# Optimization experiments

Measured on AMD Instinct MI355X. Metric: run time of the kernel, lower is better.

Reference implementation:

```python
import jax, jax.numpy as jnp
import numpy as np

D_MODEL = 2048
N_HEADS = 16
HEAD_DIM = D_MODEL // N_HEADS  # 128
ROPE_BASE = 10000.0


def _rope_cos_sin(T, hd, dtype):
    inv_freq = 1.0 / (ROPE_BASE ** (jnp.arange(0, hd, 2, dtype=jnp.float32) / hd))
    freqs = jnp.arange(T, dtype=jnp.float32)[:, None] * inv_freq[None, :]  # [T, hd/2]
    emb = jnp.concatenate([freqs, freqs], axis=-1)  # [T, hd]
    return jnp.cos(emb).astype(dtype), jnp.sin(emb).astype(dtype)


def _rotate_half(x):
    h = x.shape[-1] // 2
    return jnp.concatenate([-x[..., h:], x[..., :h]], axis=-1)


def setup_inputs() -> dict:
    key = jax.random.key(0)
    k1, k2, k3, k4 = jax.random.split(key, 4)
    B, T = 2, 2048
    x = jax.random.normal(k1, (B, T, D_MODEL), dtype=jnp.float32)
    # Linear weights stored as [in, out] so y = x @ W (same math as torch's x @ W.T)
    Wqkv = jax.random.normal(k2, (D_MODEL, 3 * D_MODEL), dtype=jnp.float32) * (D_MODEL ** -0.5)
    Wproj = jax.random.normal(k3, (D_MODEL, D_MODEL), dtype=jnp.float32) * (D_MODEL ** -0.5)
    bproj = jax.random.normal(k4, (D_MODEL,), dtype=jnp.float32) * 0.01
    # additive causal mask: 0 on/below diagonal, -1e9 above
    causal = jnp.tril(jnp.ones((T, T), dtype=bool))
    mask = jnp.where(causal, 0.0, -1e9).astype(jnp.float32)
    return {"x": x, "Wqkv": Wqkv, "Wproj": Wproj, "bproj": bproj, "mask": mask}


def reference(x, Wqkv, Wproj, bproj, mask):
    B, T, D = x.shape
    H, hd = N_HEADS, HEAD_DIM
    scale = hd ** -0.5

    qkv = x @ Wqkv  # [B, T, 3D]
    q, k, v = jnp.split(qkv, 3, axis=-1)
    q = q.reshape(B, T, H, hd).transpose(0, 2, 1, 3)  # [B, H, T, hd]
    k = k.reshape(B, T, H, hd).transpose(0, 2, 1, 3)
    v = v.reshape(B, T, H, hd).transpose(0, 2, 1, 3)

    cos, sin = _rope_cos_sin(T, hd, x.dtype)  # [T, hd]
    q = q * cos + _rotate_half(q) * sin
    k = k * cos + _rotate_half(k) * sin

    attn = jnp.einsum('bhtd,bhsd->bhts', q, k) * scale  # [B, H, T, T]
    attn = attn + mask  # broadcast [T, T] over (B, H)
    attn = jax.nn.softmax(attn, axis=-1)
    out = jnp.einsum('bhts,bhsd->bhtd', attn, v)  # [B, H, T, hd]
    out = out.transpose(0, 2, 1, 3).reshape(B, T, D)
    return out @ Wproj + bproj
```

## Files before the change

### kernel.cpp

```cpp
#include <hip/hip_runtime.h>
#include <cstdint>

#define BB 2
#define TT 2048
#define DM 2048
#define NH 16
#define HD 128
#define QKVN 6144

using f32x4   = __attribute__((ext_vector_type(4))) float;
using bf16x8  = __attribute__((ext_vector_type(8))) __bf16;
using ushort8 = __attribute__((ext_vector_type(8))) unsigned short;

static __device__ __forceinline__ unsigned short f2bf(float f) {
    uint32_t u = __builtin_bit_cast(uint32_t, f);
    u += 0x7FFFu + ((u >> 16) & 1u);
    return (unsigned short)(u >> 16);
}
static __device__ __forceinline__ float bf2f(unsigned short h) {
    return __builtin_bit_cast(float, ((uint32_t)h) << 16);
}

#define GLOAD16(SRC, DST)                                               \
    __builtin_amdgcn_global_load_lds(                                   \
        (const __attribute__((address_space(1))) void*)(SRC),           \
        (__attribute__((address_space(3))) void*)(DST), 16, 0, 0)

__global__ __launch_bounds__(256) void k_split(const float* __restrict__ in,
                                               unsigned short* __restrict__ hi,
                                               unsigned short* __restrict__ lo,
                                               int n4) {
    int i = blockIdx.x * 256 + threadIdx.x;
    if (i >= n4) return;
    float4 v = reinterpret_cast<const float4*>(in)[i];
    ushort4 h, l;
    h.x = f2bf(v.x); l.x = f2bf(v.x - bf2f(h.x));
    h.y = f2bf(v.y); l.y = f2bf(v.y - bf2f(h.y));
    h.z = f2bf(v.z); l.z = f2bf(v.z - bf2f(h.z));
    h.w = f2bf(v.w); l.w = f2bf(v.w - bf2f(h.w));
    reinterpret_cast<ushort4*>(hi)[i] = h;
    reinterpret_cast<ushort4*>(lo)[i] = l;
}

__global__ __launch_bounds__(256) void k_tsplit(const float* __restrict__ W,
                                                unsigned short* __restrict__ th,
                                                int K, int N) {
    __shared__ float tile[32][33];
    int bn = blockIdx.x * 32, bk = blockIdx.y * 32;
    int tx = threadIdx.x, ty = threadIdx.y;
#pragma unroll
    for (int r = 0; r < 4; r++)
        tile[ty + 8 * r][tx] = W[(size_t)(bk + ty + 8 * r) * N + bn + tx];
    __syncthreads();
#pragma unroll
    for (int r = 0; r < 4; r++) {
        float v = tile[tx][ty + 8 * r];
        int row = bn + ty + 8 * r, col = bk + tx;
        th[(size_t)row * K + col] = f2bf(v);
    }
}

template <int EPI>
__global__ __launch_bounds__(512, 2) void k_gemm(
    const unsigned short* __restrict__ Ah, const unsigned short* __restrict__ Al,
    const unsigned short* __restrict__ Bh,
    unsigned short* __restrict__ Ch,
    float* __restrict__ Cf, const float* __restrict__ bias,
    int M, int N, int K) {
    __shared__ __align__(16) unsigned short sAh[2][16384];
    __shared__ __align__(16) unsigned short sAl[2][16384];
    __shared__ __align__(16) unsigned short sBh[2][8192];

    const int nwg = gridDim.x * gridDim.y;
    const int L = blockIdx.y * gridDim.x + blockIdx.x;
    const int logical = (L & 7) * (nwg >> 3) + (L >> 3);
    const int bx = logical % gridDim.x, by = logical / gridDim.x;

    const int tid = threadIdx.x;
    const int wave = tid >> 6, lane = tid & 63;
    const int g = lane >> 4, r16 = lane & 15;
    const int arow0 = by * 256, bcol0 = bx * 128;
    const int wr = (wave >> 1) * 64, wc = (wave & 1) * 64;
    const int sw8 = r16 & 7;

    const int srow = tid >> 3;
    const int scol = ((tid & 7) ^ (srow & 7)) << 3;

    f32x4 acc[4][4];
#pragma unroll
    for (int m = 0; m < 4; m++)
#pragma unroll
        for (int n = 0; n < 4; n++) acc[m][n] = (f32x4){0.f, 0.f, 0.f, 0.f};

    const int NT = K >> 6;

    auto stageA_hi = [&](int buf, int tk) {
        const size_t kof = (size_t)tk * 64 + scol;
#pragma unroll
        for (int i = 0; i < 4; i++)
            GLOAD16(Ah + (size_t)(arow0 + i * 64 + srow) * K + kof,
                    &sAh[buf][(i * 512 + tid) * 8]);
    };
    auto stageA_lo = [&](int buf, int tk) {
        const size_t kof = (size_t)tk * 64 + scol;
#pragma unroll
        for (int i = 0; i < 4; i++)
            GLOAD16(Al + (size_t)(arow0 + i * 64 + srow) * K + kof,
                    &sAl[buf][(i * 512 + tid) * 8]);
    };
    auto stageB = [&](int buf, int tk) {
        const size_t kof = (size_t)tk * 64 + scol;
#pragma unroll
        for (int i = 0; i < 2; i++)
            GLOAD16(Bh + (size_t)(bcol0 + i * 64 + srow) * K + kof,
                    &sBh[buf][(i * 512 + tid) * 8]);
    };

    auto rdA = [&](int buf, int m, int co, bf16x8& h, bf16x8& l) {
        int ro = (wr + m * 16 + r16) * 64 + co;
        h = __builtin_bit_cast(bf16x8, *(const ushort8*)&sAh[buf][ro]);
        l = __builtin_bit_cast(bf16x8, *(const ushort8*)&sAl[buf][ro]);
    };
    auto rdB = [&](int buf, int n, int co) {
        int ro = (wc + n * 16 + r16) * 64 + co;
        return __builtin_bit_cast(bf16x8, *(const ushort8*)&sBh[buf][ro]);
    };

    stageA_hi(0, 0); stageA_lo(0, 0); stageB(0, 0);

    int cur = 0;
    for (int t = 0; t < NT; ++t) {
        asm volatile("s_waitcnt vmcnt(0)" ::: "memory");
        __builtin_amdgcn_s_barrier();
        const bool pf = (t + 1 < NT);
        const int nb = cur ^ 1;
        const int co0 = (g ^ sw8) << 3, co1 = ((4 + g) ^ sw8) << 3;

        bf16x8 ah0[4], al0[4], bh0[4], ah1[4], al1[4], bh1[4];

#pragma unroll
        for (int n = 0; n < 4; n++) bh0[n] = rdB(cur, n, co0);
        rdA(cur, 0, co0, ah0[0], al0[0]);
        rdA(cur, 1, co0, ah0[1], al0[1]);
        __builtin_amdgcn_sched_barrier(0);
        rdA(cur, 2, co0, ah0[2], al0[2]);
        rdA(cur, 3, co0, ah0[3], al0[3]);
        __builtin_amdgcn_sched_barrier(0);
        if (pf) stageA_hi(nb, t + 1);
        asm volatile("s_waitcnt lgkmcnt(4)" ::: "memory");
        __builtin_amdgcn_sched_barrier(0);
        __builtin_amdgcn_s_setprio(1);
#pragma unroll
        for (int m = 0; m < 2; m++)
#pragma unroll
            for (int n = 0; n < 4; n++) {
                acc[m][n] = __builtin_amdgcn_mfma_f32_16x16x32_bf16(ah0[m], bh0[n], acc[m][n], 0, 0, 0);
                acc[m][n] = __builtin_amdgcn_mfma_f32_16x16x32_bf16(al0[m], bh0[n], acc[m][n], 0, 0, 0);
            }
        __builtin_amdgcn_s_setprio(0);
        __builtin_amdgcn_s_barrier();

        rdA(cur, 0, co1, ah1[0], al1[0]);
        rdA(cur, 1, co1, ah1[1], al1[1]);
        __builtin_amdgcn_sched_barrier(0);
        if (pf) stageA_lo(nb, t + 1);
        asm volatile("s_waitcnt lgkmcnt(4)" ::: "memory");
        __builtin_amdgcn_sched_barrier(0);
        __builtin_amdgcn_s_setprio(1);
#pragma unroll
        for (int m = 2; m < 4; m++)
#pragma unroll
            for (int n = 0; n < 4; n++) {
                acc[m][n] = __builtin_amdgcn_mfma_f32_16x16x32_bf16(ah0[m], bh0[n], acc[m][n], 0, 0, 0);
                acc[m][n] = __builtin_amdgcn_mfma_f32_16x16x32_bf16(al0[m], bh0[n], acc[m][n], 0, 0, 0);
            }
        __builtin_amdgcn_s_setprio(0);
        __builtin_amdgcn_s_barrier();

#pragma unroll
        for (int n = 0; n < 4; n++) bh1[n] = rdB(cur, n, co1);
        __builtin_amdgcn_sched_barrier(0);
        rdA(cur, 2, co1, ah1[2], al1[2]);
        rdA(cur, 3, co1, ah1[3], al1[3]);
        __builtin_amdgcn_sched_barrier(0);
        if (pf) stageB(nb, t + 1);
        asm volatile("s_waitcnt lgkmcnt(4)" ::: "memory");
        __builtin_amdgcn_sched_barrier(0);
        __builtin_amdgcn_s_setprio(1);
#pragma unroll
        for (int m = 0; m < 2; m++)
#pragma unroll
            for (int n = 0; n < 4; n++) {
                acc[m][n] = __builtin_amdgcn_mfma_f32_16x16x32_bf16(ah1[m], bh1[n], acc[m][n], 0, 0, 0);
                acc[m][n] = __builtin_amdgcn_mfma_f32_16x16x32_bf16(al1[m], bh1[n], acc[m][n], 0, 0, 0);
            }
        __builtin_amdgcn_s_setprio(0);
        __builtin_amdgcn_s_barrier();

        asm volatile("s_waitcnt lgkmcnt(0)" ::: "memory");
        __builtin_amdgcn_sched_barrier(0);
        __builtin_amdgcn_s_setprio(1);
#pragma unroll
        for (int m = 2; m < 4; m++)
#pragma unroll
            for (int n = 0; n < 4; n++) {
                acc[m][n] = __builtin_amdgcn_mfma_f32_16x16x32_bf16(ah1[m], bh1[n], acc[m][n], 0, 0, 0);
                acc[m][n] = __builtin_amdgcn_mfma_f32_16x16x32_bf16(al1[m], bh1[n], acc[m][n], 0, 0, 0);
            }
        __builtin_amdgcn_s_setprio(0);
        cur ^= 1;
    }

#pragma unroll
    for (int m = 0; m < 4; m++)
#pragma unroll
        for (int n = 0; n < 4; n++) {
            int col = bcol0 + wc + n * 16 + r16;
#pragma unroll
            for (int j = 0; j < 4; j++) {
                int row = arow0 + wr + m * 16 + g * 4 + j;
                float v = acc[m][n][j];
                if (EPI == 0) {
                    Ch[(size_t)row * N + col] = f2bf(v);
                } else {
                    Cf[(size_t)row * N + col] = v + bias[col];
                }
            }
        }
}

__global__ __launch_bounds__(256) void k_rope(unsigned short* __restrict__ qh) {
    __shared__ float row[4096];
    __shared__ float cs[64], sn[64];
    const int rb = blockIdx.x;
    const int t = rb & (TT - 1);
    const int tid = threadIdx.x;
    if (tid < 64) {
        float invf = 1.0f / powf(10000.0f, (float)tid * (1.0f / 64.0f));
        float s, c;
        sincosf((float)t * invf, &s, &c);
        cs[tid] = c; sn[tid] = s;
    }
    const size_t base = (size_t)rb * QKVN;
#pragma unroll
    for (int i = 0; i < 2; i++) {
        int c0 = (tid + i * 256) * 8;
        ushort8 h = *(const ushort8*)&qh[base + c0];
#pragma unroll
        for (int e = 0; e < 8; e++) row[c0 + e] = bf2f(h[e]);
    }
    __syncthreads();
#pragma unroll
    for (int i = 0; i < 2; i++) {
        int c0 = (tid + i * 256) * 8;
        int d0 = c0 & 127;
        ushort8 h;
#pragma unroll
        for (int e = 0; e < 8; e++) {
            int c = c0 + e, d = d0 + e;
            float x = row[c];
            float xr = (d < 64) ? -row[c + 64] : row[c - 64];
            float v = x * cs[d & 63] + xr * sn[d & 63];
            h[e] = f2bf(v);
        }
        *(ushort8*)&qh[base + c0] = h;
    }
}

__global__ __launch_bounds__(128) void k_vt(const unsigned short* __restrict__ qkvh,
                                            unsigned short* __restrict__ vt) {
    const int bh = blockIdx.x;
    const int tc = blockIdx.y;
    const int d = threadIdx.x;
    const int b = bh >> 4, h = bh & 15;
    unsigned short buf[64];
    const size_t src0 = ((size_t)(b * TT + tc * 64)) * QKVN + 4096 + h * 128 + d;
#pragma unroll
    for (int ttt = 0; ttt < 64; ttt++) buf[ttt] = qkvh[src0 + (size_t)ttt * QKVN];
    const size_t dst = ((size_t)bh * 128 + d) * TT + tc * 64;
#pragma unroll
    for (int i = 0; i < 8; i++)
        *(ushort8*)&vt[dst + i * 8] = *(const ushort8*)&buf[i * 8];
}

__global__ __launch_bounds__(256) void k_flash(const unsigned short* __restrict__ qkvh,
                                               const unsigned short* __restrict__ vt,
                                               unsigned short* __restrict__ aoh,
                                               unsigned short* __restrict__ aol) {
    __shared__ unsigned short sK[2][64 * 128];
    __shared__ unsigned short sV[2][128 * 64];
    __shared__ unsigned short sP[4][16 * 64];

    const int L = blockIdx.y * gridDim.x + blockIdx.x;
    const int logical = (L & 7) * 128 + (L >> 3);
    const int bh = logical >> 5;
    const int qb = 31 - (logical & 31);
    const int b = bh >> 4, h = bh & 15;

    const int tid = threadIdx.x, wave = tid >> 6, lane = tid & 63;
    const int g = lane >> 4, r16 = lane & 15;
    const float scale = 0.08838834764831845f;

    bf16x8 qf[4];
    {
        const int qrow = qb * 64 + wave * 16 + r16;
        const size_t qbase = ((size_t)(b * TT) + qrow) * QKVN + h * 128;
#pragma unroll
        for (int kk = 0; kk < 4; kk++) {
            ushort8 u = *(const ushort8*)&qkvh[qbase + kk * 32 + g * 8];
            ushort8 o;
#pragma unroll
            for (int e = 0; e < 8; e++) o[e] = f2bf(bf2f(u[e]) * scale);
            qf[kk] = __builtin_bit_cast(bf16x8, o);
        }
    }

    f32x4 oacc[8];
#pragma unroll
    for (int n = 0; n < 8; n++) oacc[n] = (f32x4){0.f, 0.f, 0.f, 0.f};
    float mrun[4], lrun[4];
#pragma unroll
    for (int j = 0; j < 4; j++) { mrun[j] = -1e30f; lrun[j] = 0.f; }

    const int k_row_st = wave * 4 + (lane >> 4);
    const int v_row_st = wave * 8 + (lane >> 3);
    const int lidx = wave * 512 + lane * 8;

    auto stage = [&](int buf, int kb) {
#pragma unroll
        for (int i = 0; i < 4; i++) {
            int krow = i * 16 + k_row_st;
            int kcol = ((lane & 15) ^ (krow & 7)) << 3;
            GLOAD16(qkvh + ((size_t)(b * TT + kb * 64 + krow)) * QKVN + 2048 + h * 128 + kcol,
                    &sK[buf][i * 2048 + lidx]);
            int vrow = i * 32 + v_row_st;
            int vcol = ((lane & 7) ^ (vrow & 7)) << 3;
            GLOAD16(vt + ((size_t)bh * 128 + vrow) * TT + kb * 64 + vcol,
                    &sV[buf][i * 2048 + lidx]);
        }
    };

    const int nkb = qb + 1;
    int cur = 0;
    stage(0, 0);

    for (int kb = 0; kb < nkb; kb++) {
        __syncthreads();
        if (kb + 1 < nkb) stage(cur ^ 1, kb + 1);

        f32x4 sacc[4];
#pragma unroll
        for (int n = 0; n < 4; n++) sacc[n] = (f32x4){0.f, 0.f, 0.f, 0.f};
#pragma unroll
        for (int n = 0; n < 4; n++) {
            const int krow = n * 16 + r16;
            const int rbase = krow * 128;
            const int sw = krow & 7;
#pragma unroll
            for (int kk = 0; kk < 4; kk++) {
                int slot = (kk * 4 + g) ^ sw;
                bf16x8 kf = __builtin_bit_cast(bf16x8, *(const ushort8*)&sK[cur][rbase + slot * 8]);
                sacc[n] = __builtin_amdgcn_mfma_f32_16x16x32_bf16(qf[kk], kf, sacc[n], 0, 0, 0);
            }
        }

        const int key0 = kb * 64;
#pragma unroll
        for (int j = 0; j < 4; j++) {
            const int prow = g * 4 + j;
            const int qg = qb * 64 + wave * 16 + prow;
            float s0 = sacc[0][j], s1 = sacc[1][j], s2 = sacc[2][j], s3 = sacc[3][j];
            if (kb == qb) {
                if (key0 + r16 > qg)      s0 = -1e30f;
                if (key0 + 16 + r16 > qg) s1 = -1e30f;
                if (key0 + 32 + r16 > qg) s2 = -1e30f;
                if (key0 + 48 + r16 > qg) s3 = -1e30f;
            }
            float tmax = fmaxf(fmaxf(s0, s1), fmaxf(s2, s3));
#pragma unroll
            for (int off = 8; off >= 1; off >>= 1) tmax = fmaxf(tmax, __shfl_xor(tmax, off));
            float mnew = fmaxf(mrun[j], tmax);
            float corr = __expf(mrun[j] - mnew);
            float p0 = __expf(s0 - mnew), p1 = __expf(s1 - mnew);
            float p2 = __expf(s2 - mnew), p3 = __expf(s3 - mnew);
            float rs = (p0 + p1) + (p2 + p3);
#pragma unroll
            for (int off = 8; off >= 1; off >>= 1) rs += __shfl_xor(rs, off);
            lrun[j] = lrun[j] * corr + rs;
            mrun[j] = mnew;
#pragma unroll
            for (int n = 0; n < 8; n++) oacc[n][j] *= corr;
            const int pb = prow * 64, sw = prow & 7, e = r16 & 7, hi2 = (r16 >> 3);
            sP[wave][pb + (((0 + hi2) ^ sw) << 3) + e] = f2bf(p0);
            sP[wave][pb + (((2 + hi2) ^ sw) << 3) + e] = f2bf(p1);
            sP[wave][pb + (((4 + hi2) ^ sw) << 3) + e] = f2bf(p2);
            sP[wave][pb + (((6 + hi2) ^ sw) << 3) + e] = f2bf(p3);
        }

#pragma unroll
        for (int kk = 0; kk < 2; kk++) {
            const int slot = (kk * 4 + g) ^ (r16 & 7);
            bf16x8 pf = __builtin_bit_cast(bf16x8, *(const ushort8*)&sP[wave][r16 * 64 + slot * 8]);
#pragma unroll
            for (int n = 0; n < 8; n++) {
                const int d = n * 16 + r16;
                bf16x8 vf = __builtin_bit_cast(bf16x8, *(const ushort8*)&sV[cur][d * 64 + slot * 8]);
                oacc[n] = __builtin_amdgcn_mfma_f32_16x16x32_bf16(pf, vf, oacc[n], 0, 0, 0);
            }
        }
        cur ^= 1;
    }

#pragma unroll
    for (int j = 0; j < 4; j++) {
        float inv = 1.0f / lrun[j];
        int qg = qb * 64 + wave * 16 + g * 4 + j;
        size_t obase = ((size_t)(b * TT) + qg) * DM + h * 128;
#pragma unroll
        for (int n = 0; n < 8; n++) {
            float v = oacc[n][j] * inv;
            unsigned short hh = f2bf(v);
            aoh[obase + n * 16 + r16] = hh;
            aol[obase + n * 16 + r16] = f2bf(v - bf2f(hh));
        }
    }
}

extern "C" void kernel_launch(void* const* d_in, const int* in_sizes, int n_in,
                              void* d_out, int out_size, void* d_ws, size_t ws_size,
                              hipStream_t stream) {
    const float* x = (const float*)d_in[0];
    const float* Wqkv = (const float*)d_in[1];
    const float* Wproj = (const float*)d_in[2];
    const float* bproj = (const float*)d_in[3];

    uint8_t* w = (uint8_t*)d_ws;
    auto alloc = [&](size_t bytes) { uint8_t* p = w; w += bytes; return p; };
    unsigned short* xh   = (unsigned short*)alloc(8388608ull * 2);
    unsigned short* xl   = (unsigned short*)alloc(8388608ull * 2);
    unsigned short* wqh  = (unsigned short*)alloc(12582912ull * 2);
    unsigned short* wph  = (unsigned short*)alloc(4194304ull * 2);
    unsigned short* qkvh = (unsigned short*)alloc(25165824ull * 2);
    unsigned short* vtp  = (unsigned short*)alloc(8388608ull * 2);
    unsigned short* aoh  = (unsigned short*)alloc(8388608ull * 2);
    unsigned short* aol  = (unsigned short*)alloc(8388608ull * 2);

    k_split<<<dim3(8192), dim3(256), 0, stream>>>(x, xh, xl, 2097152);
    k_tsplit<<<dim3(192, 64), dim3(32, 8), 0, stream>>>(Wqkv, wqh, 2048, 6144);
    k_tsplit<<<dim3(64, 64), dim3(32, 8), 0, stream>>>(Wproj, wph, 2048, 2048);
    k_gemm<0><<<dim3(48, 16), dim3(512), 0, stream>>>(xh, xl, wqh,
                                                      qkvh, nullptr, nullptr,
                                                      4096, 6144, 2048);
    k_rope<<<dim3(4096), dim3(256), 0, stream>>>(qkvh);
    k_vt<<<dim3(32, 32), dim3(128), 0, stream>>>(qkvh, vtp);
    k_flash<<<dim3(32, 32), dim3(256), 0, stream>>>(qkvh, vtp, aoh, aol);
    k_gemm<1><<<dim3(16, 16), dim3(512), 0, stream>>>(aoh, aol, wph,
                                                      nullptr, (float*)d_out, bproj,
                                                      4096, 2048, 2048);
}
```

Before: 559.6 us.

## Load GEMM A operand directly to registers and drop lo-split for projection

The GEMM no longer stages the A operand (hi/lo bf16 halves) through LDS. Each wave loads its A fragments straight from global memory into registers, one k-tile ahead, and only B stays double-buffered in shared memory. Most intra-iteration barriers are removed and the vmcnt waits are relaxed. Separately, the attention output is written only as a single bf16 (no lo residual), and the output projection GEMM runs without the split term, halving its MFMA work. The risks are lower accuracy in the projection and uncoalesced per-lane global loads for A, with more register pressure.

```diff
diff --git a/kernel.cpp b/kernel.cpp
--- a/kernel.cpp
+++ b/kernel.cpp
@@ -60,15 +60,13 @@
     }
 }
 
-template <int EPI>
+template <int EPI, int SPLIT>
 __global__ __launch_bounds__(512, 2) void k_gemm(
     const unsigned short* __restrict__ Ah, const unsigned short* __restrict__ Al,
     const unsigned short* __restrict__ Bh,
     unsigned short* __restrict__ Ch,
     float* __restrict__ Cf, const float* __restrict__ bias,
     int M, int N, int K) {
-    __shared__ __align__(16) unsigned short sAh[2][16384];
-    __shared__ __align__(16) unsigned short sAl[2][16384];
     __shared__ __align__(16) unsigned short sBh[2][8192];
 
     const int nwg = gridDim.x * gridDim.y;
@@ -86,6 +84,11 @@
     const int srow = tid >> 3;
     const int scol = ((tid & 7) ^ (srow & 7)) << 3;
 
+    size_t aBase[4];
+#pragma unroll
+    for (int m = 0; m < 4; m++)
+        aBase[m] = (size_t)(arow0 + wr + m * 16 + r16) * K + g * 8;
+
     f32x4 acc[4][4];
 #pragma unroll
     for (int m = 0; m < 4; m++)
@@ -94,20 +97,6 @@
 
     const int NT = K >> 6;
 
-    auto stageA_hi = [&](int buf, int tk) {
-        const size_t kof = (size_t)tk * 64 + scol;
-#pragma unroll
-        for (int i = 0; i < 4; i++)
-            GLOAD16(Ah + (size_t)(arow0 + i * 64 + srow) * K + kof,
-                    &sAh[buf][(i * 512 + tid) * 8]);
-    };
-    auto stageA_lo = [&](int buf, int tk) {
-        const size_t kof = (size_t)tk * 64 + scol;
-#pragma unroll
-        for (int i = 0; i < 4; i++)
-            GLOAD16(Al + (size_t)(arow0 + i * 64 + srow) * K + kof,
-                    &sAl[buf][(i * 512 + tid) * 8]);
-    };
     auto stageB = [&](int buf, int tk) {
         const size_t kof = (size_t)tk * 64 + scol;
 #pragma unroll
@@ -115,99 +104,97 @@
             GLOAD16(Bh + (size_t)(bcol0 + i * 64 + srow) * K + kof,
                     &sBh[buf][(i * 512 + tid) * 8]);
     };
-
-    auto rdA = [&](int buf, int m, int co, bf16x8& h, bf16x8& l) {
-        int ro = (wr + m * 16 + r16) * 64 + co;
-        h = __builtin_bit_cast(bf16x8, *(const ushort8*)&sAh[buf][ro]);
-        l = __builtin_bit_cast(bf16x8, *(const ushort8*)&sAl[buf][ro]);
-    };
-    auto rdB = [&](int buf, int n, int co) {
-        int ro = (wc + n * 16 + r16) * 64 + co;
+    auto rdB = [&](int buf, int n, int slot) {
+        int ro = (wc + n * 16 + r16) * 64 + ((slot ^ sw8) << 3);
         return __builtin_bit_cast(bf16x8, *(const ushort8*)&sBh[buf][ro]);
     };
 
-    stageA_hi(0, 0); stageA_lo(0, 0); stageB(0, 0);
+    bf16x8 a0h[4], a0l[4], a1h[4], a1l[4];
+    auto loadA0 = [&](int kcol) {
+#pragma unroll
+        for (int m = 0; m < 4; m++) {
+            a0h[m] = __builtin_bit_cast(bf16x8, *(const ushort8*)(Ah + aBase[m] + kcol));
+            if (SPLIT) a0l[m] = __builtin_bit_cast(bf16x8, *(const ushort8*)(Al + aBase[m] + kcol));
+        }
+    };
+    auto loadA1 = [&](int kcol) {
+#pragma unroll
+        for (int m = 0; m < 4; m++) {
+            a1h[m] = __builtin_bit_cast(bf16x8, *(const ushort8*)(Ah + aBase[m] + kcol + 32));
+            if (SPLIT) a1l[m] = __builtin_bit_cast(bf16x8, *(const ushort8*)(Al + aBase[m] + kcol + 32));
+        }
+    };
+
+    stageB(0, 0);
+    loadA0(0);
+    loadA1(0);
 
     int cur = 0;
     for (int t = 0; t < NT; ++t) {
-        asm volatile("s_waitcnt vmcnt(0)" ::: "memory");
+        if (SPLIT) asm volatile("s_waitcnt vmcnt(16)" ::: "memory");
+        else       asm volatile("s_waitcnt vmcnt(8)" ::: "memory");
         __builtin_amdgcn_s_barrier();
         const bool pf = (t + 1 < NT);
         const int nb = cur ^ 1;
-        const int co0 = (g ^ sw8) << 3, co1 = ((4 + g) ^ sw8) << 3;
-
-        bf16x8 ah0[4], al0[4], bh0[4], ah1[4], al1[4], bh1[4];
-
-#pragma unroll
-        for (int n = 0; n < 4; n++) bh0[n] = rdB(cur, n, co0);
-        rdA(cur, 0, co0, ah0[0], al0[0]);
-        rdA(cur, 1, co0, ah0[1], al0[1]);
-        __builtin_amdgcn_sched_barrier(0);
-        rdA(cur, 2, co0, ah0[2], al0[2]);
-        rdA(cur, 3, co0, ah0[3], al0[3]);
-        __builtin_amdgcn_sched_barrier(0);
-        if (pf) stageA_hi(nb, t + 1);
-        asm volatile("s_waitcnt lgkmcnt(4)" ::: "memory");
+        const int nkcol = (t + 1) * 64;
+
+        bf16x8 bh0[4], bh1[4];
+#pragma unroll
+        for (int n = 0; n < 4; n++) bh0[n] = rdB(cur, n, g);
+#pragma unroll
+        for (int n = 0; n < 4; n++) bh1[n] = rdB(cur, n, 4 + g);
+        if (pf) stageB(nb, t + 1);
         __builtin_amdgcn_sched_barrier(0);
         __builtin_amdgcn_s_setprio(1);
 #pragma unroll
         for (int m = 0; m < 2; m++)
 #pragma unroll
             for (int n = 0; n < 4; n++) {
-                acc[m][n] = __builtin_amdgcn_mfma_f32_16x16x32_bf16(ah0[m], bh0[n], acc[m][n], 0, 0, 0);
-                acc[m][n] = __builtin_amdgcn_mfma_f32_16x16x32_bf16(al0[m], bh0[n], acc[m][n], 0, 0, 0);
+                acc[m][n] = __builtin_amdgcn_mfma_f32_16x16x32_bf16(a0h[m], bh0[n], acc[m][n], 0, 0, 0);
+                if (SPLIT)
+                    acc[m][n] = __builtin_amdgcn_mfma_f32_16x16x32_bf16(a0l[m], bh0[n], acc[m][n], 0, 0, 0);
             }
         __builtin_amdgcn_s_setprio(0);
-        __builtin_amdgcn_s_barrier();
-
-        rdA(cur, 0, co1, ah1[0], al1[0]);
-        rdA(cur, 1, co1, ah1[1], al1[1]);
-        __builtin_amdgcn_sched_barrier(0);
-        if (pf) stageA_lo(nb, t + 1);
-        asm volatile("s_waitcnt lgkmcnt(4)" ::: "memory");
-        __builtin_amdgcn_sched_barrier(0);
+        __builtin_amdgcn_sched_barrier(0);
+
         __builtin_amdgcn_s_setprio(1);
 #pragma unroll
         for (int m = 2; m < 4; m++)
 #pragma unroll
             for (int n = 0; n < 4; n++) {
-                acc[m][n] = __builtin_amdgcn_mfma_f32_16x16x32_bf16(ah0[m], bh0[n], acc[m][n], 0, 0, 0);
-                acc[m][n] = __builtin_amdgcn_mfma_f32_16x16x32_bf16(al0[m], bh0[n], acc[m][n], 0, 0, 0);
+                acc[m][n] = __builtin_amdgcn_mfma_f32_16x16x32_bf16(a0h[m], bh0[n], acc[m][n], 0, 0, 0);
+                if (SPLIT)
+                    acc[m][n] = __builtin_amdgcn_mfma_f32_16x16x32_bf16(a0l[m], bh0[n], acc[m][n], 0, 0, 0);
             }
         __builtin_amdgcn_s_setprio(0);
-        __builtin_amdgcn_s_barrier();
-
-#pragma unroll
-        for (int n = 0; n < 4; n++) bh1[n] = rdB(cur, n, co1);
-        __builtin_amdgcn_sched_barrier(0);
-        rdA(cur, 2, co1, ah1[2], al1[2]);
-        rdA(cur, 3, co1, ah1[3], al1[3]);
-        __builtin_amdgcn_sched_barrier(0);
-        if (pf) stageB(nb, t + 1);
-        asm volatile("s_waitcnt lgkmcnt(4)" ::: "memory");
+        __builtin_amdgcn_sched_barrier(0);
+
+        if (pf) loadA0(nkcol);
         __builtin_amdgcn_sched_barrier(0);
         __builtin_amdgcn_s_setprio(1);
 #pragma unroll
         for (int m = 0; m < 2; m++)
 #pragma unroll
             for (int n = 0; n < 4; n++) {
-                acc[m][n] = __builtin_amdgcn_mfma_f32_16x16x32_bf16(ah1[m], bh1[n], acc[m][n], 0, 0, 0);
-                acc[m][n] = __builtin_amdgcn_mfma_f32_16x16x32_bf16(al1[m], bh1[n], acc[m][n], 0, 0, 0);
+                acc[m][n] = __builtin_amdgcn_mfma_f32_16x16x32_bf16(a1h[m], bh1[n], acc[m][n], 0, 0, 0);
+                if (SPLIT)
+                    acc[m][n] = __builtin_amdgcn_mfma_f32_16x16x32_bf16(a1l[m], bh1[n], acc[m][n], 0, 0, 0);
             }
         __builtin_amdgcn_s_setprio(0);
-        __builtin_amdgcn_s_barrier();
-
-        asm volatile("s_waitcnt lgkmcnt(0)" ::: "memory");
-        __builtin_amdgcn_sched_barrier(0);
+        __builtin_amdgcn_sched_barrier(0);
+
         __builtin_amdgcn_s_setprio(1);
 #pragma unroll
         for (int m = 2; m < 4; m++)
 #pragma unroll
             for (int n = 0; n < 4; n++) {
-                acc[m][n] = __builtin_amdgcn_mfma_f32_16x16x32_bf16(ah1[m], bh1[n], acc[m][n], 0, 0, 0);
-                acc[m][n] = __builtin_amdgcn_mfma_f32_16x16x32_bf16(al1[m], bh1[n], acc[m][n], 0, 0, 0);
+                acc[m][n] = __builtin_amdgcn_mfma_f32_16x16x32_bf16(a1h[m], bh1[n], acc[m][n], 0, 0, 0);
+                if (SPLIT)
+                    acc[m][n] = __builtin_amdgcn_mfma_f32_16x16x32_bf16(a1l[m], bh1[n], acc[m][n], 0, 0, 0);
             }
         __builtin_amdgcn_s_setprio(0);
+        __builtin_amdgcn_sched_barrier(0);
+        if (pf) loadA1(nkcol);
         cur ^= 1;
     }
 
@@ -285,8 +272,7 @@
 
 __global__ __launch_bounds__(256) void k_flash(const unsigned short* __restrict__ qkvh,
                                                const unsigned short* __restrict__ vt,
-                                               unsigned short* __restrict__ aoh,
-                                               unsigned short* __restrict__ aol) {
+                                               unsigned short* __restrict__ aoh) {
     __shared__ unsigned short sK[2][64 * 128];
     __shared__ unsigned short sV[2][128 * 64];
     __shared__ unsigned short sP[4][16 * 64];
@@ -417,12 +403,8 @@
         int qg = qb * 64 + wave * 16 + g * 4 + j;
         size_t obase = ((size_t)(b * TT) + qg) * DM + h * 128;
 #pragma unroll
-        for (int n = 0; n < 8; n++) {
-            float v = oacc[n][j] * inv;
-            unsigned short hh = f2bf(v);
-            aoh[obase + n * 16 + r16] = hh;
-            aol[obase + n * 16 + r16] = f2bf(v - bf2f(hh));
-        }
+        for (int n = 0; n < 8; n++)
+            aoh[obase + n * 16 + r16] = f2bf(oacc[n][j] * inv);
     }
 }
 
@@ -443,18 +425,17 @@
     unsigned short* qkvh = (unsigned short*)alloc(25165824ull * 2);
     unsigned short* vtp  = (unsigned short*)alloc(8388608ull * 2);
     unsigned short* aoh  = (unsigned short*)alloc(8388608ull * 2);
-    unsigned short* aol  = (unsigned short*)alloc(8388608ull * 2);
 
     k_split<<<dim3(8192), dim3(256), 0, stream>>>(x, xh, xl, 2097152);
     k_tsplit<<<dim3(192, 64), dim3(32, 8), 0, stream>>>(Wqkv, wqh, 2048, 6144);
     k_tsplit<<<dim3(64, 64), dim3(32, 8), 0, stream>>>(Wproj, wph, 2048, 2048);
-    k_gemm<0><<<dim3(48, 16), dim3(512), 0, stream>>>(xh, xl, wqh,
-                                                      qkvh, nullptr, nullptr,
-                                                      4096, 6144, 2048);
+    k_gemm<0, 1><<<dim3(48, 16), dim3(512), 0, stream>>>(xh, xl, wqh,
+                                                         qkvh, nullptr, nullptr,
+                                                         4096, 6144, 2048);
     k_rope<<<dim3(4096), dim3(256), 0, stream>>>(qkvh);
     k_vt<<<dim3(32, 32), dim3(128), 0, stream>>>(qkvh, vtp);
-    k_flash<<<dim3(32, 32), dim3(256), 0, stream>>>(qkvh, vtp, aoh, aol);
-    k_gemm<1><<<dim3(16, 16), dim3(512), 0, stream>>>(aoh, aol, wph,
-                                                      nullptr, (float*)d_out, bproj,
-                                                      4096, 2048, 2048);
-}
+    k_flash<<<dim3(32, 32), dim3(256), 0, stream>>>(qkvh, vtp, aoh);
+    k_gemm<1, 0><<<dim3(16, 16), dim3(512), 0, stream>>>(aoh, nullptr, wph,
+                                                         nullptr, (float*)d_out, bproj,
+                                                         4096, 2048, 2048);
+}
```

Result: slower. 799.2 us (+42.8%).
